# Optimization experiments

Measured on AMD Instinct MI355X. Metric: run time of the kernel, lower is better.

## Reference

```python
import jax, jax.numpy as jnp
import numpy as np

D_MODEL = 1024
NHEAD = 16
D_HEAD = D_MODEL // NHEAD


def setup_inputs() -> dict:
    key = jax.random.key(0)
    ks = jax.random.split(key, 9)
    B, S = 2, 2048
    scale = 1.0 / np.sqrt(D_MODEL)
    x = jax.random.normal(ks[0], (B, S, D_MODEL), dtype=jnp.float32)
    Wq = jax.random.normal(ks[1], (D_MODEL, D_MODEL), dtype=jnp.float32) * scale
    Wk = jax.random.normal(ks[2], (D_MODEL, D_MODEL), dtype=jnp.float32) * scale
    Wv = jax.random.normal(ks[3], (D_MODEL, D_MODEL), dtype=jnp.float32) * scale
    Wo = jax.random.normal(ks[4], (D_MODEL, D_MODEL), dtype=jnp.float32) * scale
    bq = jax.random.normal(ks[5], (D_MODEL,), dtype=jnp.float32) * 0.01
    bk = jax.random.normal(ks[6], (D_MODEL,), dtype=jnp.float32) * 0.01
    bv = jax.random.normal(ks[7], (D_MODEL,), dtype=jnp.float32) * 0.01
    bo = jax.random.normal(ks[8], (D_MODEL,), dtype=jnp.float32) * 0.01
    return {"x": x, "Wq": Wq, "bq": bq, "Wk": Wk, "bk": bk,
            "Wv": Wv, "bv": bv, "Wo": Wo, "bo": bo}


def reference(x, Wq, bq, Wk, bk, Wv, bv, Wo, bo):
    B, S, D = x.shape
    H, Dh = NHEAD, D_HEAD
    # projections; weights stored as (in, out) so y = x @ W + b
    def split_heads(t):  # [B,S,D] -> [B,H,S,Dh]
        return t.reshape(B, S, H, Dh).transpose(0, 2, 1, 3)
    q = split_heads(x @ Wq + bq)
    k = split_heads(x @ Wk + bk)
    v = split_heads(x @ Wv + bv)
    scale = 1.0 / jnp.sqrt(jnp.asarray(Dh, dtype=x.dtype))
    attn = jnp.einsum("bhqd,bhkd->bhqk", q, k) * scale  # [B,H,S,S]
    attn = jax.nn.softmax(attn, axis=-1)
    out = jnp.einsum("bhqk,bhkd->bhqd", attn, v)  # [B,H,S,Dh]
    out = out.transpose(0, 2, 1, 3).reshape(B, S, D)
    return out @ Wo + bo
```

## Files before the change

kernel.cpp:

```cpp
#include <hip/hip_runtime.h>
#include <hip/hip_bf16.h>
#include <stdint.h>
#include <stddef.h>

typedef __bf16 b16;
typedef __bf16 b16x4 __attribute__((ext_vector_type(4)));
typedef __bf16 b16x8 __attribute__((ext_vector_type(8)));
typedef float  f32x4 __attribute__((ext_vector_type(4)));

#define LOG2E 1.4426950408889634f
#define QSCALE (0.125f * LOG2E)

#if __has_builtin(__builtin_amdgcn_exp2f)
#define EXP2F(x) __builtin_amdgcn_exp2f(x)
#else
#define EXP2F(x) exp2f(x)
#endif

typedef __attribute__((address_space(1))) void gvoid;
typedef __attribute__((address_space(3))) void svoid;

__device__ __forceinline__ void async_cp16(void* lds, const void* g) {
    __builtin_amdgcn_global_load_lds((gvoid*)(void*)g, (svoid*)lds, 16, 0, 0);
}

__global__ __launch_bounds__(256) void k_cvt_x(const float* __restrict__ x,
                                               b16* __restrict__ xb) {
    int i = (blockIdx.x * 256 + threadIdx.x) * 4;
    float4 v = *(const float4*)(x + i);
    b16x4 o = { (b16)v.x, (b16)v.y, (b16)v.z, (b16)v.w };
    *(b16x4*)(xb + i) = o;
}

__global__ __launch_bounds__(256) void k_transpose(const float* __restrict__ Wq,
                                                   const float* __restrict__ Wk,
                                                   const float* __restrict__ Wv,
                                                   const float* __restrict__ Wo,
                                                   b16* __restrict__ WtQKV,
                                                   b16* __restrict__ Wot) {
    __shared__ float t[32][33];
    const int z = blockIdx.z;
    const float* W = (z == 0) ? Wq : (z == 1) ? Wk : (z == 2) ? Wv : Wo;
    const int k0 = blockIdx.x * 32, n0 = blockIdx.y * 32;
    const int tr = threadIdx.x >> 3, tc4 = (threadIdx.x & 7) * 4;
    float4 v = *(const float4*)(W + (size_t)(k0 + tr) * 1024 + n0 + tc4);
    t[tr][tc4 + 0] = v.x; t[tr][tc4 + 1] = v.y;
    t[tr][tc4 + 2] = v.z; t[tr][tc4 + 3] = v.w;
    __syncthreads();
    b16* dst = (z < 3) ? (WtQKV + ((size_t)z << 20)) : Wot;
    b16x4 o = { (b16)t[tc4 + 0][tr], (b16)t[tc4 + 1][tr],
                (b16)t[tc4 + 2][tr], (b16)t[tc4 + 3][tr] };
    *(b16x4*)(dst + (size_t)(n0 + tr) * 1024 + k0 + tc4) = o;
}

__device__ __forceinline__ void gemm128_core(const b16* __restrict__ Ab,
                                             const b16* __restrict__ Bb,
                                             b16* As, b16* Bs, int tid,
                                             f32x4 acc[4][4]) {
    const int lane = tid & 63, wave = tid >> 6;
    const int wm = wave & 1, wn = wave >> 1;
    const int quad = lane >> 4, lc = lane & 15;
    const int ci0 = tid, ci1 = tid + 256;
    for (int k0 = 0; k0 < 1024; k0 += 32) {
        __syncthreads();
        async_cp16(As + ci0 * 8, Ab + (ci0 >> 2) * 1024 + k0 + (ci0 & 3) * 8);
        async_cp16(As + ci1 * 8, Ab + (ci1 >> 2) * 1024 + k0 + (ci1 & 3) * 8);
        async_cp16(Bs + ci0 * 8, Bb + (ci0 >> 2) * 1024 + k0 + (ci0 & 3) * 8);
        async_cp16(Bs + ci1 * 8, Bb + (ci1 >> 2) * 1024 + k0 + (ci1 & 3) * 8);
        __syncthreads();
        b16x8 af[4], bfr[4];
#pragma unroll
        for (int mt = 0; mt < 4; ++mt)
            af[mt] = *(const b16x8*)(As + (wm * 64 + mt * 16 + lc) * 32 + quad * 8);
#pragma unroll
        for (int nt = 0; nt < 4; ++nt)
            bfr[nt] = *(const b16x8*)(Bs + (wn * 64 + nt * 16 + lc) * 32 + quad * 8);
#pragma unroll
        for (int mt = 0; mt < 4; ++mt)
#pragma unroll
            for (int nt = 0; nt < 4; ++nt)
                acc[mt][nt] = __builtin_amdgcn_mfma_f32_16x16x32_bf16(
                    af[mt], bfr[nt], acc[mt][nt], 0, 0, 0);
    }
}

__global__ __launch_bounds__(256, 2) void k_gemm_qkv(
    const b16* __restrict__ A, const b16* __restrict__ Bt,
    const float* __restrict__ bq, const float* __restrict__ bk,
    const float* __restrict__ bv,
    b16* __restrict__ Qg, b16* __restrict__ Kg, b16* __restrict__ Vtg) {
    __shared__ __align__(16) b16 As[128 * 32];
    __shared__ __align__(16) b16 Bs[128 * 32];
    const int bm = blockIdx.x, bn = blockIdx.y;
    const int tid = threadIdx.x;
    const int lane = tid & 63, wave = tid >> 6;
    const int wm = wave & 1, wn = wave >> 1;
    const int quad = lane >> 4, lc = lane & 15;

    f32x4 acc[4][4] = {};
    gemm128_core(A + (size_t)(bm * 128) * 1024, Bt + (size_t)(bn * 128) * 1024,
                 As, Bs, tid, acc);

    const int mat = bn >> 3;
    const float* bp = (mat == 0) ? bq : (mat == 1) ? bk : bv;
#pragma unroll
    for (int nt = 0; nt < 4; ++nt) {
        const int n = bn * 128 + wn * 64 + nt * 16 + lc;
        const int cm = n & 1023;
        const int h = cm >> 6, dh = cm & 63;
        const float bval = bp[cm];
#pragma unroll
        for (int mt = 0; mt < 4; ++mt) {
            const int m0 = bm * 128 + wm * 64 + mt * 16 + quad * 4;
            const int b = m0 >> 11;
            const int bh = b * 16 + h;
            const int s0 = m0 & 2047;
            if (mat == 2) {
                b16x4 o;
#pragma unroll
                for (int r = 0; r < 4; ++r) o[r] = (b16)(acc[mt][nt][r] + bval);
                *(b16x4*)(Vtg + (size_t)(bh * 64 + dh) * 2048 + s0) = o;
            } else if (mat == 0) {
#pragma unroll
                for (int r = 0; r < 4; ++r)
                    Qg[(size_t)(bh * 2048 + s0 + r) * 64 + dh] =
                        (b16)((acc[mt][nt][r] + bval) * QSCALE);
            } else {
#pragma unroll
                for (int r = 0; r < 4; ++r)
                    Kg[(size_t)(bh * 2048 + s0 + r) * 64 + dh] =
                        (b16)(acc[mt][nt][r] + bval);
            }
        }
    }
}

__device__ __forceinline__ void flash_stage(b16* Kd, b16* Vd,
                                            const b16* __restrict__ Kbh,
                                            const b16* __restrict__ Vbh,
                                            int kt, int tid) {
#pragma unroll
    for (int i = 0; i < 2; ++i) {
        const int ci = tid + i * 256;
        const int r = ci >> 3, cs = ci & 7;
        const int gc = cs ^ (r & 7);
        async_cp16(Kd + ci * 8, Kbh + (size_t)(kt * 64 + r) * 64 + gc * 8);
        async_cp16(Vd + ci * 8, Vbh + (size_t)r * 2048 + kt * 64 + gc * 8);
    }
}

__global__ __launch_bounds__(256, 2) void k_flash(
    const b16* __restrict__ Qg, const b16* __restrict__ Kg,
    const b16* __restrict__ Vtg,
    float* __restrict__ Opart, float* __restrict__ lpart,
    b16* __restrict__ AO, int ktiles, int direct, int np) {
    __shared__ __align__(16) b16 Ks[2 * 64 * 64];
    __shared__ __align__(16) b16 Vs[2 * 64 * 64];
    __shared__ __align__(16) b16 Ps[256 * 64];

    const int bid = blockIdx.x;
    const int gstride = np << 5;
    const int qb = bid / gstride;
    const int rem = bid - qb * gstride;
    const int bh = rem / np;
    const int part = rem - bh * np;

    const int tid = threadIdx.x, lane = tid & 63, wave = tid >> 6;
    const int quad = lane >> 4, lc = lane & 15;

    const b16* Kbh = Kg + (size_t)bh * 2048 * 64;
    const b16* Vbh = Vtg + (size_t)bh * 64 * 2048;
    const int kt0 = part * ktiles, ktE = kt0 + ktiles;

    flash_stage(Ks, Vs, Kbh, Vbh, kt0, tid);

    const b16* Qbase = Qg + ((size_t)bh * 2048 + qb * 256 + wave * 64) * 64;
    b16x8 qf[4][2];
#pragma unroll
    for (int qt = 0; qt < 4; ++qt)
#pragma unroll
        for (int ch = 0; ch < 2; ++ch)
            qf[qt][ch] = *(const b16x8*)(Qbase + (qt * 16 + lc) * 64 + ch * 32 + quad * 8);

    f32x4 oacc[4][4] = {};
    float lsum[4] = {0.f, 0.f, 0.f, 0.f};
    b16* Pw = Ps + wave * 4096;

    for (int kt = kt0; kt < ktE; ++kt) {
        const int cur = (kt - kt0) & 1;
        const b16* Kc = Ks + cur * 4096;
        const b16* Vc = Vs + cur * 4096;

        if (kt + 1 < ktE) {
            flash_stage(Ks + (cur ^ 1) * 4096, Vs + (cur ^ 1) * 4096,
                        Kbh, Vbh, kt + 1, tid);
            asm volatile("s_waitcnt vmcnt(4)" ::: "memory");
        } else {
            asm volatile("s_waitcnt vmcnt(0)" ::: "memory");
        }
        __builtin_amdgcn_s_barrier();
        __builtin_amdgcn_sched_barrier(0);

#pragma unroll
        for (int m = 0; m < 4; ++m) {
            b16x8 kf[2];
#pragma unroll
            for (int ch = 0; ch < 2; ++ch) {
                const int row = m * 16 + lc;
                const int chunk = (ch * 4 + quad) ^ (row & 7);
                kf[ch] = *(const b16x8*)(Kc + row * 64 + chunk * 8);
            }
#pragma unroll
            for (int qt = 0; qt < 4; ++qt) {
                f32x4 s = {};
                __builtin_amdgcn_s_setprio(1);
                s = __builtin_amdgcn_mfma_f32_16x16x32_bf16(kf[0], qf[qt][0], s, 0, 0, 0);
                s = __builtin_amdgcn_mfma_f32_16x16x32_bf16(kf[1], qf[qt][1], s, 0, 0, 0);
                __builtin_amdgcn_s_setprio(0);
                float e0 = EXP2F(s[0]), e1 = EXP2F(s[1]);
                float e2 = EXP2F(s[2]), e3 = EXP2F(s[3]);
                lsum[qt] += (e0 + e1) + (e2 + e3);
                b16x4 p = { (b16)e0, (b16)e1, (b16)e2, (b16)e3 };
                const int prow = qt * 16 + lc;
                const int pbyte = (prow * 128 + m * 32 + quad * 8) ^ ((prow & 7) << 4);
                *(b16x4*)((char*)Pw + pbyte) = p;
            }
        }

#pragma unroll
        for (int ks = 0; ks < 2; ++ks) {
            b16x8 vf[4], pf[4];
#pragma unroll
            for (int dt = 0; dt < 4; ++dt) {
                const int row = dt * 16 + lc;
                const int chunk = (ks * 4 + quad) ^ (row & 7);
                vf[dt] = *(const b16x8*)(Vc + row * 64 + chunk * 8);
            }
#pragma unroll
            for (int mt = 0; mt < 4; ++mt) {
                const int prow = mt * 16 + lc;
                const int pbyte = (prow * 128 + ks * 64 + quad * 16) ^ ((prow & 7) << 4);
                pf[mt] = *(const b16x8*)((const char*)Pw + pbyte);
            }
            __builtin_amdgcn_s_setprio(1);
#pragma unroll
            for (int mt = 0; mt < 4; ++mt)
#pragma unroll
                for (int dt = 0; dt < 4; ++dt)
                    oacc[mt][dt] = __builtin_amdgcn_mfma_f32_16x16x32_bf16(
                        pf[mt], vf[dt], oacc[mt][dt], 0, 0, 0);
            __builtin_amdgcn_s_setprio(0);
        }

        __builtin_amdgcn_sched_barrier(0);
        __builtin_amdgcn_s_barrier();
    }

#pragma unroll
    for (int qt = 0; qt < 4; ++qt) {
        lsum[qt] += __shfl_xor(lsum[qt], 16, 64);
        lsum[qt] += __shfl_xor(lsum[qt], 32, 64);
    }

    if (!direct) {
        float* Op = Opart + ((size_t)(part * 32 + bh) * 2048 + qb * 256 + wave * 64) * 64;
#pragma unroll
        for (int mt = 0; mt < 4; ++mt)
#pragma unroll
            for (int dt = 0; dt < 4; ++dt)
#pragma unroll
                for (int r = 0; r < 4; ++r)
                    Op[(mt * 16 + quad * 4 + r) * 64 + dt * 16 + lc] = oacc[mt][dt][r];
        if (quad == 0) {
            float* lp = lpart + (size_t)(part * 32 + bh) * 2048 + qb * 256 + wave * 64;
#pragma unroll
            for (int qt = 0; qt < 4; ++qt) lp[qt * 16 + lc] = lsum[qt];
        }
    } else {
        float* Ls = (float*)(void*)Pw;
        if (quad == 0) {
#pragma unroll
            for (int qt = 0; qt < 4; ++qt) Ls[qt * 16 + lc] = lsum[qt];
        }
        const int b = bh >> 4, h = bh & 15;
#pragma unroll
        for (int mt = 0; mt < 4; ++mt)
#pragma unroll
            for (int r = 0; r < 4; ++r) {
                const float inv = 1.0f / Ls[mt * 16 + quad * 4 + r];
                const int s = qb * 256 + wave * 64 + mt * 16 + quad * 4 + r;
#pragma unroll
                for (int dt = 0; dt < 4; ++dt)
                    AO[(size_t)(b * 2048 + s) * 1024 + h * 64 + dt * 16 + lc] =
                        (b16)(oacc[mt][dt][r] * inv);
            }
    }
}

__global__ __launch_bounds__(256) void k_merge(const float* __restrict__ Opart,
                                               const float* __restrict__ lpart,
                                               b16* __restrict__ AO, int np) {
    const int bh = blockIdx.y;
    const int q = blockIdx.x * 16 + (threadIdx.x >> 4);
    const int d4 = (threadIdx.x & 15) * 4;
    const size_t qi = (size_t)bh * 2048 + q;
    f32x4 o = *(const f32x4*)(Opart + qi * 64 + d4);
    float l = lpart[qi];
    if (np == 2) {
        o += *(const f32x4*)(Opart + (qi + (size_t)32 * 2048) * 64 + d4);
        l += lpart[qi + (size_t)32 * 2048];
    }
    const float inv = 1.0f / l;
    const int b = bh >> 4, h = bh & 15;
    b16x4 ob = { (b16)(o[0] * inv), (b16)(o[1] * inv),
                 (b16)(o[2] * inv), (b16)(o[3] * inv) };
    *(b16x4*)(AO + (size_t)(b * 2048 + q) * 1024 + h * 64 + d4) = ob;
}

__global__ __launch_bounds__(256, 2) void k_gemm_out(
    const b16* __restrict__ A, const b16* __restrict__ Bt,
    const float* __restrict__ bo, float* __restrict__ out) {
    __shared__ __align__(16) b16 As[128 * 32];
    __shared__ __align__(16) b16 Bs[128 * 32];
    const int bm = blockIdx.x, bn = blockIdx.y;
    const int tid = threadIdx.x;
    const int lane = tid & 63, wave = tid >> 6;
    const int wm = wave & 1, wn = wave >> 1;
    const int quad = lane >> 4, lc = lane & 15;

    f32x4 acc[4][4] = {};
    gemm128_core(A + (size_t)(bm * 128) * 1024, Bt + (size_t)(bn * 128) * 1024,
                 As, Bs, tid, acc);

#pragma unroll
    for (int nt = 0; nt < 4; ++nt) {
        const int n = bn * 128 + wn * 64 + nt * 16 + lc;
        const float bval = bo[n];
#pragma unroll
        for (int mt = 0; mt < 4; ++mt) {
            const int m0 = bm * 128 + wm * 64 + mt * 16 + quad * 4;
#pragma unroll
            for (int r = 0; r < 4; ++r)
                out[(size_t)(m0 + r) * 1024 + n] = acc[mt][nt][r] + bval;
        }
    }
}

extern "C" void kernel_launch(void* const* d_in, const int* in_sizes, int n_in,
                              void* d_out, int out_size, void* d_ws, size_t ws_size,
                              hipStream_t stream) {
    const float* x  = (const float*)d_in[0];
    const float* Wq = (const float*)d_in[1];
    const float* bq = (const float*)d_in[2];
    const float* Wk = (const float*)d_in[3];
    const float* bk = (const float*)d_in[4];
    const float* Wv = (const float*)d_in[5];
    const float* bv = (const float*)d_in[6];
    const float* Wo = (const float*)d_in[7];
    const float* bo = (const float*)d_in[8];
    float* out = (float*)d_out;

    char* ws = (char*)d_ws;
    const size_t MB = 1024 * 1024;
    b16* Xb  = (b16*)(ws);
    b16* AO  = (b16*)(ws);
    b16* WtQ = (b16*)(ws + 8 * MB);
    b16* Wot = (b16*)(ws + 14 * MB);
    b16* Qg  = (b16*)(ws + 16 * MB);
    b16* Kg  = (b16*)(ws + 24 * MB);
    b16* Vtg = (b16*)(ws + 32 * MB);

    const size_t need2 = 40 * MB + 2 * (16 * MB) + 2 * 256 * 1024;
    const int np = (ws_size >= need2) ? 2 : 1;
    float* Opart = (float*)(ws + 40 * MB);
    float* lpart = (float*)(ws + 40 * MB + (size_t)np * 16 * MB);
    const int direct = (np == 1);

    k_cvt_x<<<4096, 256, 0, stream>>>(x, Xb);
    k_transpose<<<dim3(32, 32, 4), 256, 0, stream>>>(Wq, Wk, Wv, Wo, WtQ, Wot);
    k_gemm_qkv<<<dim3(32, 24), 256, 0, stream>>>(Xb, WtQ, bq, bk, bv, Qg, Kg, Vtg);
    k_flash<<<dim3(8 * 32 * np), 256, 0, stream>>>(Qg, Kg, Vtg, Opart, lpart, AO,
                                                   32 / np, direct, np);
    if (!direct)
        k_merge<<<dim3(128, 32), 256, 0, stream>>>(Opart, lpart, AO, np);
    k_gemm_out<<<dim3(32, 8), 256, 0, stream>>>(AO, Wot, bo, out);
}
```

Before: 196.0 us.

## Keep softmax probabilities in registers and halve flash query tile per block

The flash kernel permutes the key rows of the QK^T MFMA so that its output fragments already match the A-operand layout of the PV MFMA. This removes the LDS store and reload of P. Each block now covers 128 queries instead of 256, which doubles the grid and raises launch bounds to 4 blocks per CU. The LDS swizzle is changed to match the new key access pattern. The trade-off is that K/V tiles are reloaded across twice as many blocks, adding L2 traffic, in exchange for less LDS use and higher occupancy.

```diff
diff --git a/kernel.cpp b/kernel.cpp
--- a/kernel.cpp
+++ b/kernel.cpp
@@ -23,6 +23,8 @@
 __device__ __forceinline__ void async_cp16(void* lds, const void* g) {
     __builtin_amdgcn_global_load_lds((gvoid*)(void*)g, (svoid*)lds, 16, 0, 0);
 }
+
+#define SW(r) ((((r) & 7)) ^ (((r) >> 1) & 4))
 
 __global__ __launch_bounds__(256) void k_cvt_x(const float* __restrict__ x,
                                                b16* __restrict__ xb) {
@@ -143,20 +145,20 @@
     for (int i = 0; i < 2; ++i) {
         const int ci = tid + i * 256;
         const int r = ci >> 3, cs = ci & 7;
-        const int gc = cs ^ (r & 7);
+        const int gc = cs ^ SW(r);
         async_cp16(Kd + ci * 8, Kbh + (size_t)(kt * 64 + r) * 64 + gc * 8);
         async_cp16(Vd + ci * 8, Vbh + (size_t)r * 2048 + kt * 64 + gc * 8);
     }
 }
 
-__global__ __launch_bounds__(256, 2) void k_flash(
+__global__ __launch_bounds__(256, 4) void k_flash(
     const b16* __restrict__ Qg, const b16* __restrict__ Kg,
     const b16* __restrict__ Vtg,
     float* __restrict__ Opart, float* __restrict__ lpart,
     b16* __restrict__ AO, int ktiles, int direct, int np) {
     __shared__ __align__(16) b16 Ks[2 * 64 * 64];
     __shared__ __align__(16) b16 Vs[2 * 64 * 64];
-    __shared__ __align__(16) b16 Ps[256 * 64];
+    __shared__ float Lred[4][32];
 
     const int bid = blockIdx.x;
     const int gstride = np << 5;
@@ -174,17 +176,16 @@
 
     flash_stage(Ks, Vs, Kbh, Vbh, kt0, tid);
 
-    const b16* Qbase = Qg + ((size_t)bh * 2048 + qb * 256 + wave * 64) * 64;
-    b16x8 qf[4][2];
-#pragma unroll
-    for (int qt = 0; qt < 4; ++qt)
+    const b16* Qbase = Qg + ((size_t)bh * 2048 + qb * 128 + wave * 32) * 64;
+    b16x8 qf[2][2];
+#pragma unroll
+    for (int qt = 0; qt < 2; ++qt)
 #pragma unroll
         for (int ch = 0; ch < 2; ++ch)
             qf[qt][ch] = *(const b16x8*)(Qbase + (qt * 16 + lc) * 64 + ch * 32 + quad * 8);
 
-    f32x4 oacc[4][4] = {};
-    float lsum[4] = {0.f, 0.f, 0.f, 0.f};
-    b16* Pw = Ps + wave * 4096;
+    f32x4 oacc[2][4] = {};
+    float lsum[2] = {0.f, 0.f};
 
     for (int kt = kt0; kt < ktE; ++kt) {
         const int cur = (kt - kt0) & 1;
@@ -202,53 +203,47 @@
         __builtin_amdgcn_sched_barrier(0);
 
 #pragma unroll
-        for (int m = 0; m < 4; ++m) {
-            b16x8 kf[2];
-#pragma unroll
-            for (int ch = 0; ch < 2; ++ch) {
-                const int row = m * 16 + lc;
-                const int chunk = (ch * 4 + quad) ^ (row & 7);
-                kf[ch] = *(const b16x8*)(Kc + row * 64 + chunk * 8);
+        for (int ks = 0; ks < 2; ++ks) {
+            b16x8 pf[2];
+#pragma unroll
+            for (int t = 0; t < 2; ++t) {
+                const int krow = ks * 32 + (lc >> 2) * 8 + t * 4 + (lc & 3);
+                b16x8 kf[2];
+#pragma unroll
+                for (int ch = 0; ch < 2; ++ch) {
+                    const int slot = (ch * 4 + quad) ^ SW(krow);
+                    kf[ch] = *(const b16x8*)(Kc + krow * 64 + slot * 8);
+                }
+#pragma unroll
+                for (int qt = 0; qt < 2; ++qt) {
+                    f32x4 s = {};
+                    __builtin_amdgcn_s_setprio(1);
+                    s = __builtin_amdgcn_mfma_f32_16x16x32_bf16(kf[0], qf[qt][0], s, 0, 0, 0);
+                    s = __builtin_amdgcn_mfma_f32_16x16x32_bf16(kf[1], qf[qt][1], s, 0, 0, 0);
+                    __builtin_amdgcn_s_setprio(0);
+                    float e0 = EXP2F(s[0]), e1 = EXP2F(s[1]);
+                    float e2 = EXP2F(s[2]), e3 = EXP2F(s[3]);
+                    lsum[qt] += (e0 + e1) + (e2 + e3);
+                    pf[qt][t * 4 + 0] = (b16)e0;
+                    pf[qt][t * 4 + 1] = (b16)e1;
+                    pf[qt][t * 4 + 2] = (b16)e2;
+                    pf[qt][t * 4 + 3] = (b16)e3;
+                }
             }
-#pragma unroll
-            for (int qt = 0; qt < 4; ++qt) {
-                f32x4 s = {};
-                __builtin_amdgcn_s_setprio(1);
-                s = __builtin_amdgcn_mfma_f32_16x16x32_bf16(kf[0], qf[qt][0], s, 0, 0, 0);
-                s = __builtin_amdgcn_mfma_f32_16x16x32_bf16(kf[1], qf[qt][1], s, 0, 0, 0);
-                __builtin_amdgcn_s_setprio(0);
-                float e0 = EXP2F(s[0]), e1 = EXP2F(s[1]);
-                float e2 = EXP2F(s[2]), e3 = EXP2F(s[3]);
-                lsum[qt] += (e0 + e1) + (e2 + e3);
-                b16x4 p = { (b16)e0, (b16)e1, (b16)e2, (b16)e3 };
-                const int prow = qt * 16 + lc;
-                const int pbyte = (prow * 128 + m * 32 + quad * 8) ^ ((prow & 7) << 4);
-                *(b16x4*)((char*)Pw + pbyte) = p;
-            }
-        }
-
-#pragma unroll
-        for (int ks = 0; ks < 2; ++ks) {
-            b16x8 vf[4], pf[4];
+            b16x8 vf[4];
 #pragma unroll
             for (int dt = 0; dt < 4; ++dt) {
                 const int row = dt * 16 + lc;
-                const int chunk = (ks * 4 + quad) ^ (row & 7);
-                vf[dt] = *(const b16x8*)(Vc + row * 64 + chunk * 8);
-            }
-#pragma unroll
-            for (int mt = 0; mt < 4; ++mt) {
-                const int prow = mt * 16 + lc;
-                const int pbyte = (prow * 128 + ks * 64 + quad * 16) ^ ((prow & 7) << 4);
-                pf[mt] = *(const b16x8*)((const char*)Pw + pbyte);
+                const int slot = (ks * 4 + quad) ^ SW(row);
+                vf[dt] = *(const b16x8*)(Vc + row * 64 + slot * 8);
             }
             __builtin_amdgcn_s_setprio(1);
 #pragma unroll
-            for (int mt = 0; mt < 4; ++mt)
+            for (int qt = 0; qt < 2; ++qt)
 #pragma unroll
                 for (int dt = 0; dt < 4; ++dt)
-                    oacc[mt][dt] = __builtin_amdgcn_mfma_f32_16x16x32_bf16(
-                        pf[mt], vf[dt], oacc[mt][dt], 0, 0, 0);
+                    oacc[qt][dt] = __builtin_amdgcn_mfma_f32_16x16x32_bf16(
+                        pf[qt], vf[dt], oacc[qt][dt], 0, 0, 0);
             __builtin_amdgcn_s_setprio(0);
         }
 
@@ -257,42 +252,41 @@
     }
 
 #pragma unroll
-    for (int qt = 0; qt < 4; ++qt) {
+    for (int qt = 0; qt < 2; ++qt) {
         lsum[qt] += __shfl_xor(lsum[qt], 16, 64);
         lsum[qt] += __shfl_xor(lsum[qt], 32, 64);
     }
 
     if (!direct) {
-        float* Op = Opart + ((size_t)(part * 32 + bh) * 2048 + qb * 256 + wave * 64) * 64;
-#pragma unroll
-        for (int mt = 0; mt < 4; ++mt)
+        float* Op = Opart + ((size_t)(part * 32 + bh) * 2048 + qb * 128 + wave * 32) * 64;
+#pragma unroll
+        for (int qt = 0; qt < 2; ++qt)
 #pragma unroll
             for (int dt = 0; dt < 4; ++dt)
 #pragma unroll
                 for (int r = 0; r < 4; ++r)
-                    Op[(mt * 16 + quad * 4 + r) * 64 + dt * 16 + lc] = oacc[mt][dt][r];
+                    Op[(qt * 16 + quad * 4 + r) * 64 + dt * 16 + lc] = oacc[qt][dt][r];
         if (quad == 0) {
-            float* lp = lpart + (size_t)(part * 32 + bh) * 2048 + qb * 256 + wave * 64;
-#pragma unroll
-            for (int qt = 0; qt < 4; ++qt) lp[qt * 16 + lc] = lsum[qt];
+            float* lp = lpart + (size_t)(part * 32 + bh) * 2048 + qb * 128 + wave * 32;
+#pragma unroll
+            for (int qt = 0; qt < 2; ++qt) lp[qt * 16 + lc] = lsum[qt];
         }
     } else {
-        float* Ls = (float*)(void*)Pw;
         if (quad == 0) {
 #pragma unroll
-            for (int qt = 0; qt < 4; ++qt) Ls[qt * 16 + lc] = lsum[qt];
+            for (int qt = 0; qt < 2; ++qt) Lred[wave][qt * 16 + lc] = lsum[qt];
         }
         const int b = bh >> 4, h = bh & 15;
 #pragma unroll
-        for (int mt = 0; mt < 4; ++mt)
+        for (int qt = 0; qt < 2; ++qt)
 #pragma unroll
             for (int r = 0; r < 4; ++r) {
-                const float inv = 1.0f / Ls[mt * 16 + quad * 4 + r];
-                const int s = qb * 256 + wave * 64 + mt * 16 + quad * 4 + r;
+                const float inv = 1.0f / Lred[wave][qt * 16 + quad * 4 + r];
+                const int s = qb * 128 + wave * 32 + qt * 16 + quad * 4 + r;
 #pragma unroll
                 for (int dt = 0; dt < 4; ++dt)
                     AO[(size_t)(b * 2048 + s) * 1024 + h * 64 + dt * 16 + lc] =
-                        (b16)(oacc[mt][dt][r] * inv);
+                        (b16)(oacc[qt][dt][r] * inv);
             }
     }
 }
@@ -379,8 +373,8 @@
     k_cvt_x<<<4096, 256, 0, stream>>>(x, Xb);
     k_transpose<<<dim3(32, 32, 4), 256, 0, stream>>>(Wq, Wk, Wv, Wo, WtQ, Wot);
     k_gemm_qkv<<<dim3(32, 24), 256, 0, stream>>>(Xb, WtQ, bq, bk, bv, Qg, Kg, Vtg);
-    k_flash<<<dim3(8 * 32 * np), 256, 0, stream>>>(Qg, Kg, Vtg, Opart, lpart, AO,
-                                                   32 / np, direct, np);
+    k_flash<<<dim3(16 * 32 * np), 256, 0, stream>>>(Qg, Kg, Vtg, Opart, lpart, AO,
+                                                    32 / np, direct, np);
     if (!direct)
         k_merge<<<dim3(128, 32), 256, 0, stream>>>(Opart, lpart, AO, np);
     k_gemm_out<<<dim3(32, 8), 256, 0, stream>>>(AO, Wot, bo, out);
```

Result: no change. 197.1 us (+0.6%).
